# Kernel tuning notes

Measured on AMD Instinct MI355X. Metric: run time of the kernel, lower is better.

## Reference

```python
import jax, jax.numpy as jnp
import numpy as np

B, C, H, W = 16, 512, 32, 32
NH, HD = 8, 64
CTX_DIM, L = 768, 512
EPS = 1e-5


def setup_inputs() -> dict:
    key = jax.random.key(0)
    ks = jax.random.split(key, 10)
    x = jax.random.normal(ks[0], (B, C, H, W), dtype=jnp.float32)
    context = jax.random.normal(ks[1], (B, L, CTX_DIM), dtype=jnp.float32)
    context_mask = jax.random.randint(ks[2], (B, L), 0, 2).astype(bool)
    context_mask = context_mask.at[:, 0].set(True)  # guarantee >=1 valid key per row
    s = 0.02
    ln_w = jnp.ones((C,), jnp.float32)
    ln_b = jnp.zeros((C,), jnp.float32)
    Wq = jax.random.normal(ks[3], (C, C), jnp.float32) * s
    Wk = jax.random.normal(ks[4], (C, C), jnp.float32) * s
    Wv = jax.random.normal(ks[5], (C, C), jnp.float32) * s
    Wo = jax.random.normal(ks[6], (C, C), jnp.float32) * s
    Wctx = jax.random.normal(ks[7], (C, CTX_DIM), jnp.float32) * s
    return {"x": x, "context": context, "context_mask": context_mask,
            "ln_w": ln_w, "ln_b": ln_b, "Wq": Wq, "Wk": Wk, "Wv": Wv,
            "Wo": Wo, "Wctx": Wctx}


def _layernorm(x, w, b):
    mu = jnp.mean(x, axis=-1, keepdims=True)
    var = jnp.mean(jnp.square(x - mu), axis=-1, keepdims=True)
    return (x - mu) * jax.lax.rsqrt(var + EPS) * w + b


def reference(x, context, context_mask, ln_w, ln_b, Wq, Wk, Wv, Wo, Wctx):
    b, c, h, w = x.shape
    n = h * w
    hidden = x.reshape(b, c, n).transpose(0, 2, 1)          # [b, n, c]
    hidden_norm = _layernorm(hidden, ln_w, ln_b)
    ctx = jnp.einsum('bld,cd->blc', context, Wctx)          # context_proj

    q = jnp.einsum('bnc,ec->bne', hidden_norm, Wq).reshape(b, n, NH, HD).transpose(0, 2, 1, 3)
    k = jnp.einsum('blc,ec->ble', ctx, Wk).reshape(b, -1, NH, HD).transpose(0, 2, 1, 3)
    v = jnp.einsum('blc,ec->ble', ctx, Wv).reshape(b, -1, NH, HD).transpose(0, 2, 1, 3)

    scale = HD ** -0.5
    scores = jnp.einsum('bhnd,bhld->bhnl', q, k) * scale    # [b,H,n,L]
    mask4 = context_mask[:, None, None, :]                  # [b,1,1,L]
    scores = jnp.where(mask4, scores, -jnp.inf)
    all_invalid = ~jnp.any(mask4, axis=-1, keepdims=True)   # [b,1,1,1]
    scores = jnp.where(all_invalid, 0.0, scores)
    attn = jax.nn.softmax(scores, axis=-1)
    attn = jnp.where(mask4, attn, 0.0)
    attn = jnp.where(all_invalid, 0.0, attn)

    out = jnp.einsum('bhnl,bhld->bhnd', attn, v)            # [b,H,n,hd]
    out = out.transpose(0, 2, 1, 3).reshape(b, n, c)
    out = jnp.einsum('bnc,ec->bne', out, Wo)
    out = out + hidden
    return out.transpose(0, 2, 1).reshape(b, c, h, w)
```

## Files before the change

kernel.cpp:

```cpp
#include <hip/hip_runtime.h>

#define B_   16
#define C_   512
#define N_   1024
#define L_   512
#define CTX_ 768
#define NH_  8
#define HD_  64
#define EPS_ 1e-5f

typedef short bfrag  __attribute__((ext_vector_type(8)));
typedef short bfrag4 __attribute__((ext_vector_type(4)));
typedef float f32x4  __attribute__((ext_vector_type(4)));

__device__ __forceinline__ ushort f2bf(float f) {
  union { float f; unsigned u; } v; v.f = f;
  unsigned r = v.u + 0x7fffu + ((v.u >> 16) & 1u);
  return (ushort)(r >> 16);
}

__device__ __forceinline__ f32x4 mfma16(bfrag a, bfrag b, f32x4 c) {
  return __builtin_amdgcn_mfma_f32_16x16x32_bf16(a, b, c, 0, 0, 0);
}
__device__ __forceinline__ f32x4 mfma16k16(bfrag4 a, bfrag4 b, f32x4 c) {
  return __builtin_amdgcn_mfma_f32_16x16x16bf16_1k(a, b, c, 0, 0, 0);
}
__device__ __forceinline__ unsigned cvt_pk_bf16(float lo, float hi) {
  unsigned d;
  asm("v_cvt_pk_bf16_f32 %0, %1, %2" : "=v"(d) : "v"(lo), "v"(hi));
  return d;
}

__device__ __forceinline__ void g2l16(const ushort* g, ushort* l) {
  __builtin_amdgcn_global_load_lds(
      (const __attribute__((address_space(1))) void*)g,
      (__attribute__((address_space(3))) void*)l, 16, 0, 0);
}

__global__ __launch_bounds__(256) void cast5_kernel(
    const float* __restrict__ s0, const float* __restrict__ s1,
    const float* __restrict__ s2, const float* __restrict__ s3,
    const float* __restrict__ s4,
    ushort* __restrict__ d0, ushort* __restrict__ d1, ushort* __restrict__ d2,
    ushort* __restrict__ d3, ushort* __restrict__ d4) {
  int i = blockIdx.x * 256 + threadIdx.x;
  const float* src; ushort* dst; int off;
  if      (i < 98304)  { src = s0; dst = d0; off = i; }
  else if (i < 163840) { src = s1; dst = d1; off = i - 98304; }
  else if (i < 229376) { src = s2; dst = d2; off = i - 163840; }
  else if (i < 294912) { src = s3; dst = d3; off = i - 229376; }
  else                 { src = s4; dst = d4; off = i - 294912; }
  float4 vv = ((const float4*)src)[off];
  ushort4 o;
  o.x = f2bf(vv.x); o.y = f2bf(vv.y); o.z = f2bf(vv.z); o.w = f2bf(vv.w);
  ((ushort4*)dst)[off] = o;
}

__global__ __launch_bounds__(1024) void ln_stats(const float* __restrict__ x,
                                                 float* __restrict__ mu_out,
                                                 float* __restrict__ rs_out) {
  const int b  = blockIdx.x;
  const int n0 = blockIdx.y * 64;
  const int tid = threadIdx.x;
  const int nx = tid & 63, cg = tid >> 6;
  const float* xb = x + (size_t)b * C_ * N_;

  float s = 0.f, s2 = 0.f;
  for (int c = cg; c < C_; c += 16) {
    float v = xb[(size_t)c * N_ + n0 + nx];
    s += v; s2 += v * v;
  }
  __shared__ float red[2][16][64];
  red[0][cg][nx] = s; red[1][cg][nx] = s2;
  __syncthreads();
  if (cg == 0) {
    float ss = 0.f, ss2 = 0.f;
#pragma unroll
    for (int i = 0; i < 16; ++i) { ss += red[0][i][nx]; ss2 += red[1][i][nx]; }
    float m  = ss * (1.f / C_);
    float var = ss2 * (1.f / C_) - m * m;
    mu_out[(size_t)b * N_ + n0 + nx] = m;
    rs_out[(size_t)b * N_ + n0 + nx] = rsqrtf(var + EPS_);
  }
}

__device__ __forceinline__ void gemm_core(const ushort* __restrict__ A,
                                          const ushort* __restrict__ W,
                                          int K, ushort* la, ushort* lb,
                                          f32x4 acc[4][4],
                                          int tid, int wm, int we, int col, int rg) {
  const int lane = tid & 63, w = tid >> 6;
  const int rloc = lane >> 2, pt = lane & 3;
  const int pts = pt ^ ((rloc >> 1) & 3);
  const int qsel = (rg ^ ((col >> 1) & 3)) * 8;

  for (int k0 = 0; k0 < K; k0 += 32) {
#pragma unroll
    for (int c = 0; c < 2; ++c) {
      const int chunk = w + c * 4;
      const int row = chunk * 16 + rloc;
      g2l16(A + (size_t)row * K + k0 + pts * 8, la + chunk * 512);
      g2l16(W + (size_t)row * K + k0 + pts * 8, lb + chunk * 512);
    }
    __syncthreads();
    bfrag af[4], bf[4];
#pragma unroll
    for (int i = 0; i < 4; ++i) {
      af[i] = *(const bfrag*)&la[(wm + i * 16 + col) * 32 + qsel];
      bf[i] = *(const bfrag*)&lb[(we + i * 16 + col) * 32 + qsel];
    }
#pragma unroll
    for (int i = 0; i < 4; ++i)
#pragma unroll
      for (int j = 0; j < 4; ++j)
        acc[i][j] = mfma16(af[i], bf[j], acc[i][j]);
    __syncthreads();
  }
}

__global__ __launch_bounds__(256) void gemm_kv(const ushort* __restrict__ A,
                                               const ushort* __restrict__ Wk,
                                               const ushort* __restrict__ Wv,
                                               ushort* __restrict__ Ko,
                                               ushort* __restrict__ Vt_g) {
  __shared__ ushort la[128 * 32];
  __shared__ ushort lb[128 * 32];
  __shared__ float T[16][132];
  const int isv = blockIdx.y >> 2;
  const ushort* W = isv ? Wv : Wk;
  const int m0 = blockIdx.x * 128, e0 = (blockIdx.y & 3) * 128;
  const int tid = threadIdx.x, lane = tid & 63, w = tid >> 6;
  const int wm = (w >> 1) * 64, we = (w & 1) * 64;
  const int col = lane & 15, rg = lane >> 4;

  f32x4 acc[4][4] = {};
  gemm_core(A + (size_t)m0 * C_, W + (size_t)e0 * C_, C_, la, lb, acc, tid, wm, we, col, rg);

  if (!isv) {
#pragma unroll
    for (int i = 0; i < 4; ++i)
#pragma unroll
      for (int j = 0; j < 4; ++j)
#pragma unroll
        for (int r = 0; r < 4; ++r)
          Ko[(size_t)(m0 + wm + i * 16 + rg * 4 + r) * 512 + e0 + we + j * 16 + col] =
              f2bf(acc[i][j][r]);
  } else {
    const int b = m0 >> 9, l0 = m0 & 511;
#pragma unroll
    for (int g = 0; g < 8; ++g) {
      if ((w & 1) == (g >> 2)) {
        const int j = g & 3;
#pragma unroll
        for (int i = 0; i < 4; ++i)
          *(f32x4*)&T[col][wm + i * 16 + rg * 4] = acc[i][j];
      }
      __syncthreads();
      const int n = tid & 127;
      for (int cc = tid >> 7; cc < 16; cc += 2) {
        const int e = e0 + g * 16 + cc;
        Vt_g[((size_t)b * 512 + e) * 512 + l0 + n] = f2bf(T[cc][n]);
      }
      __syncthreads();
    }
  }
}

__global__ __launch_bounds__(256) void gemm_res(const ushort* __restrict__ A,
                                                const ushort* __restrict__ W,
                                                const float* __restrict__ x,
                                                float* __restrict__ out) {
  __shared__ ushort la[128 * 32];
  __shared__ ushort lb[128 * 32];
  __shared__ float T[16][132];
  const int m0 = blockIdx.x * 128, e0 = blockIdx.y * 128;
  const int tid = threadIdx.x, lane = tid & 63, w = tid >> 6;
  const int wm = (w >> 1) * 64, we = (w & 1) * 64;
  const int col = lane & 15, rg = lane >> 4;

  f32x4 acc[4][4] = {};
  gemm_core(A + (size_t)m0 * C_, W + (size_t)e0 * C_, C_, la, lb, acc, tid, wm, we, col, rg);

  const int b = m0 >> 10, n0l = m0 & 1023;
#pragma unroll
  for (int g = 0; g < 8; ++g) {
    if ((w & 1) == (g >> 2)) {
      const int j = g & 3;
#pragma unroll
      for (int i = 0; i < 4; ++i)
        *(f32x4*)&T[col][wm + i * 16 + rg * 4] = acc[i][j];
    }
    __syncthreads();
    const int n = tid & 127;
    for (int cc = tid >> 7; cc < 16; cc += 2) {
      const int c = e0 + g * 16 + cc;
      const size_t idx = (size_t)b * C_ * N_ + (size_t)c * N_ + n0l + n;
      out[idx] = T[cc][n] + x[idx];
    }
    __syncthreads();
  }
}

__global__ __launch_bounds__(256) void gemm_ctxlnq(
    const float* __restrict__ context, const ushort* __restrict__ Wctxb,
    ushort* __restrict__ ctxo,
    const float* __restrict__ x, const float* __restrict__ mu,
    const float* __restrict__ rs, const float* __restrict__ lnw,
    const float* __restrict__ lnb, const ushort* __restrict__ Wqb,
    ushort* __restrict__ qo) {
  __shared__ ushort la[128 * 40];
  __shared__ ushort lb[128 * 40];
  const int bid = blockIdx.x;
  const int tid = threadIdx.x, lane = tid & 63, w = tid >> 6;
  const int wm = (w >> 1) * 64, we = (w & 1) * 64;
  const int col = lane & 15, rg = lane >> 4;
  const int srow = tid >> 1, sh = (tid & 1) * 16;

  f32x4 acc[4][4] = {};

  if (bid < 256) {
    const int m0 = (bid >> 2) * 128, e0 = (bid & 3) * 128;
    const int K = CTX_;
    for (int k0 = 0; k0 < K; k0 += 32) {
      {
        const float* ap = &context[(size_t)(m0 + srow) * K + k0 + sh];
        float4 f0 = ((const float4*)ap)[0];
        float4 f1 = ((const float4*)ap)[1];
        float4 f2 = ((const float4*)ap)[2];
        float4 f3 = ((const float4*)ap)[3];
        union { int4 v; ushort u[8]; } p0, p1;
        p0.u[0] = f2bf(f0.x); p0.u[1] = f2bf(f0.y); p0.u[2] = f2bf(f0.z); p0.u[3] = f2bf(f0.w);
        p0.u[4] = f2bf(f1.x); p0.u[5] = f2bf(f1.y); p0.u[6] = f2bf(f1.z); p0.u[7] = f2bf(f1.w);
        p1.u[0] = f2bf(f2.x); p1.u[1] = f2bf(f2.y); p1.u[2] = f2bf(f2.z); p1.u[3] = f2bf(f2.w);
        p1.u[4] = f2bf(f3.x); p1.u[5] = f2bf(f3.y); p1.u[6] = f2bf(f3.z); p1.u[7] = f2bf(f3.w);
        *(int4*)&la[srow * 40 + sh]     = p0.v;
        *(int4*)&la[srow * 40 + sh + 8] = p1.v;
        const ushort* wp = &Wctxb[(size_t)(e0 + srow) * K + k0 + sh];
        *(int4*)&lb[srow * 40 + sh]     = *(const int4*)wp;
        *(int4*)&lb[srow * 40 + sh + 8] = *(const int4*)(wp + 8);
      }
      __syncthreads();
      bfrag af[4], bf[4];
#pragma unroll
      for (int i = 0; i < 4; ++i) {
        af[i] = *(const bfrag*)&la[(wm + i * 16 + col) * 40 + rg * 8];
        bf[i] = *(const bfrag*)&lb[(we + i * 16 + col) * 40 + rg * 8];
      }
#pragma unroll
      for (int i = 0; i < 4; ++i)
#pragma unroll
        for (int j = 0; j < 4; ++j)
          acc[i][j] = mfma16(af[i], bf[j], acc[i][j]);
      __syncthreads();
    }
#pragma unroll
    for (int i = 0; i < 4; ++i)
#pragma unroll
      for (int j = 0; j < 4; ++j)
#pragma unroll
        for (int r = 0; r < 4; ++r)
          ctxo[(size_t)(m0 + wm + i * 16 + rg * 4 + r) * 512 + e0 + we + j * 16 + col] =
              f2bf(acc[i][j][r]);
  } else {
    const int b2 = bid - 256;
    const int m0 = (b2 >> 2) * 128, e0 = (b2 & 3) * 128;
    const int b = m0 >> 10, n0l = m0 & 1023;
    const int nloc = tid & 127, chalf = (tid >> 7) * 16;

    const float muv = mu[(size_t)b * N_ + n0l + nloc];
    const float rsv = rs[(size_t)b * N_ + n0l + nloc];
    const float nmr = -muv * rsv;
    const float* xb = x + (size_t)b * C_ * N_ + n0l + nloc;

    for (int k0 = 0; k0 < C_; k0 += 32) {
      {
        union { int4 v[2]; ushort u[16]; } pk;
#pragma unroll
        for (int i = 0; i < 16; ++i) {
          const int c = k0 + chalf + i;
          const float xv = xb[(size_t)c * N_];
          const float t = fmaf(xv, rsv, nmr);
          pk.u[i] = f2bf(fmaf(t, lnw[c], lnb[c]));
        }
        *(int4*)&la[nloc * 40 + chalf]     = pk.v[0];
        *(int4*)&la[nloc * 40 + chalf + 8] = pk.v[1];
        const ushort* wp = &Wqb[(size_t)(e0 + srow) * C_ + k0 + sh];
        *(int4*)&lb[srow * 40 + sh]     = *(const int4*)wp;
        *(int4*)&lb[srow * 40 + sh + 8] = *(const int4*)(wp + 8);
      }
      __syncthreads();
      bfrag af[4], bf[4];
#pragma unroll
      for (int i = 0; i < 4; ++i) {
        af[i] = *(const bfrag*)&la[(wm + i * 16 + col) * 40 + rg * 8];
        bf[i] = *(const bfrag*)&lb[(we + i * 16 + col) * 40 + rg * 8];
      }
#pragma unroll
      for (int i = 0; i < 4; ++i)
#pragma unroll
        for (int j = 0; j < 4; ++j)
          acc[i][j] = mfma16(af[i], bf[j], acc[i][j]);
      __syncthreads();
    }
#pragma unroll
    for (int i = 0; i < 4; ++i)
#pragma unroll
      for (int j = 0; j < 4; ++j)
#pragma unroll
        for (int r = 0; r < 4; ++r)
          qo[(size_t)(m0 + wm + i * 16 + rg * 4 + r) * 512 + e0 + we + j * 16 + col] =
              f2bf(acc[i][j][r]);
  }
}

__global__ __launch_bounds__(256) void attn_mfma(const ushort* __restrict__ q,
                                                 const ushort* __restrict__ k,
                                                 const ushort* __restrict__ vt,
                                                 const int* __restrict__ mask,
                                                 ushort* __restrict__ o) {
  __shared__ ushort Kl[2][64 * 72];
  __shared__ ushort Vt[2][64 * 72];
  __shared__ float mlb[2][64];

  const int lin = blockIdx.x;
  const int hb = lin & 127, qb = lin >> 7;
  const int h = hb & 7, b = hb >> 3;
  const int q0 = qb * 128;
  const int tid = threadIdx.x, lane = tid & 63, w = tid >> 6;
  const int col = lane & 15, rg = lane >> 4;
  const int wq = w * 32;
  const float C1 = 0.18033688011112042f;

  bfrag qf[2][2];
#pragma unroll
  for (int mi = 0; mi < 2; ++mi)
#pragma unroll
    for (int kc = 0; kc < 2; ++kc)
      qf[mi][kc] = *(const bfrag*)
          &q[((size_t)b * N_ + q0 + wq + mi * 16 + col) * C_ + h * HD_ + kc * 32 + rg * 8];

  f32x4 oa[2][4] = {};
  float l_part[2] = {0.f, 0.f};

  {
#pragma unroll
    for (int it = 0; it < 2; ++it) {
      const int idx = it * 256 + tid;
      const int key = idx >> 3, part = idx & 7;
      *(int4*)&Kl[0][key * 72 + part * 8] =
          *(const int4*)&k[((size_t)b * L_ + key) * C_ + h * HD_ + part * 8];
    }
#pragma unroll
    for (int it = 0; it < 2; ++it) {
      const int idx = it * 256 + tid;
      const int d = idx >> 3, k8 = (idx & 7) * 8;
      *(int4*)&Vt[0][d * 72 + k8] =
          *(const int4*)&vt[((size_t)b * 512 + h * HD_ + d) * 512 + k8];
    }
    if (tid < 64) mlb[0][tid] = mask[b * L_ + tid] ? 0.f : -1e30f;
  }
  __syncthreads();

  for (int t = 0; t < 8; ++t) {
    const int cur = t & 1;
    int4 kreg[2];
    int4 vreg[2];
    float mreg = 0.f;
    if (t < 7) {
      const int l0n = (t + 1) * 64;
#pragma unroll
      for (int it = 0; it < 2; ++it) {
        const int idx = it * 256 + tid;
        const int key = idx >> 3, part = idx & 7;
        kreg[it] = *(const int4*)&k[((size_t)b * L_ + l0n + key) * C_ + h * HD_ + part * 8];
      }
#pragma unroll
      for (int it = 0; it < 2; ++it) {
        const int idx = it * 256 + tid;
        const int d = idx >> 3, k8 = (idx & 7) * 8;
        vreg[it] = *(const int4*)&vt[((size_t)b * 512 + h * HD_ + d) * 512 + l0n + k8];
      }
      if (tid < 64) mreg = mask[b * L_ + l0n + tid] ? 0.f : -1e30f;
    }

    const ushort* Kc = &Kl[cur][0];
    const ushort* Vc = &Vt[cur][0];
    f32x4 s2[2][4] = {};
#pragma unroll
    for (int kc = 0; kc < 2; ++kc) {
      bfrag kf[4];
#pragma unroll
      for (int ni = 0; ni < 4; ++ni)
        kf[ni] = *(const bfrag*)&Kc[(ni * 16 + col) * 72 + kc * 32 + rg * 8];
#pragma unroll
      for (int mi = 0; mi < 2; ++mi)
#pragma unroll
        for (int ni = 0; ni < 4; ++ni)
          s2[mi][ni] = mfma16(kf[ni], qf[mi][kc], s2[mi][ni]);
    }
    bfrag4 pf[2][4];
#pragma unroll
    for (int ni = 0; ni < 4; ++ni) {
      const f32x4 bias4 = *(const f32x4*)&mlb[cur][ni * 16 + rg * 4];
#pragma unroll
      for (int mi = 0; mi < 2; ++mi) {
        const float p0 = exp2f(fmaf(s2[mi][ni][0], C1, bias4[0]));
        const float p1 = exp2f(fmaf(s2[mi][ni][1], C1, bias4[1]));
        const float p2 = exp2f(fmaf(s2[mi][ni][2], C1, bias4[2]));
        const float p3 = exp2f(fmaf(s2[mi][ni][3], C1, bias4[3]));
        l_part[mi] += (p0 + p1) + (p2 + p3);
        union { bfrag4 v; unsigned u[2]; } pk;
        pk.u[0] = cvt_pk_bf16(p0, p1);
        pk.u[1] = cvt_pk_bf16(p2, p3);
        pf[mi][ni] = pk.v;
      }
    }
#pragma unroll
    for (int ni = 0; ni < 4; ++ni) {
      bfrag4 vf[4];
#pragma unroll
      for (int di = 0; di < 4; ++di)
        vf[di] = *(const bfrag4*)&Vc[(di * 16 + col) * 72 + ni * 16 + rg * 4];
#pragma unroll
      for (int mi = 0; mi < 2; ++mi)
#pragma unroll
        for (int di = 0; di < 4; ++di)
          oa[mi][di] = mfma16k16(pf[mi][ni], vf[di], oa[mi][di]);
    }

    if (t < 7) {
      const int nb = cur ^ 1;
#pragma unroll
      for (int it = 0; it < 2; ++it) {
        const int idx = it * 256 + tid;
        const int key = idx >> 3, part = idx & 7;
        *(int4*)&Kl[nb][key * 72 + part * 8] = kreg[it];
      }
#pragma unroll
      for (int it = 0; it < 2; ++it) {
        const int idx = it * 256 + tid;
        const int d = idx >> 3, k8 = (idx & 7) * 8;
        *(int4*)&Vt[nb][d * 72 + k8] = vreg[it];
      }
      if (tid < 64) mlb[nb][tid] = mreg;
    }
    __syncthreads();
  }

  float linv[2][4];
#pragma unroll
  for (int mi = 0; mi < 2; ++mi) {
    float l = l_part[mi];
    l += __shfl_xor(l, 16);
    l += __shfl_xor(l, 32);
#pragma unroll
    for (int r = 0; r < 4; ++r) {
      int lv = __builtin_amdgcn_ds_bpermute((rg * 4 + r) * 4, __float_as_int(l));
      linv[mi][r] = 1.f / __int_as_float(lv);
    }
  }
#pragma unroll
  for (int mi = 0; mi < 2; ++mi)
#pragma unroll
    for (int r = 0; r < 4; ++r) {
      const size_t row = (size_t)b * N_ + q0 + wq + mi * 16 + rg * 4 + r;
#pragma unroll
      for (int di = 0; di < 4; ++di)
        o[row * C_ + h * HD_ + di * 16 + col] = f2bf(oa[mi][di][r] * linv[mi][r]);
    }
}

extern "C" void kernel_launch(void* const* d_in, const int* in_sizes, int n_in,
                              void* d_out, int out_size, void* d_ws, size_t ws_size,
                              hipStream_t stream) {
  (void)in_sizes; (void)n_in; (void)out_size; (void)ws_size;
  const float* x       = (const float*)d_in[0];
  const float* context = (const float*)d_in[1];
  const int*   mask    = (const int*)d_in[2];
  const float* ln_w    = (const float*)d_in[3];
  const float* ln_b    = (const float*)d_in[4];
  const float* Wq      = (const float*)d_in[5];
  const float* Wk      = (const float*)d_in[6];
  const float* Wv      = (const float*)d_in[7];
  const float* Wo      = (const float*)d_in[8];
  const float* Wctx    = (const float*)d_in[9];

  char* wsb = (char*)d_ws;
  ushort* qb    = (ushort*)(wsb + 0);
  ushort* kb    = (ushort*)(wsb + 16777216);
  ushort* vb    = (ushort*)(wsb + 25165824);
  ushort* atto  = (ushort*)(wsb + 33554432);
  ushort* ctx   = (ushort*)(wsb + 50331648);
  ushort* wctxb = (ushort*)(wsb + 58720256);
  ushort* wqb   = (ushort*)(wsb + 59506688);
  ushort* wkb   = (ushort*)(wsb + 60030976);
  ushort* wvb   = (ushort*)(wsb + 60555264);
  ushort* wob   = (ushort*)(wsb + 61079552);
  float*  mub   = (float*)(wsb + 61603840);
  float*  rsb   = (float*)(wsb + 61669376);

  cast5_kernel<<<1408, 256, 0, stream>>>(Wctx, Wq, Wk, Wv, Wo,
                                         wctxb, wqb, wkb, wvb, wob);
  ln_stats<<<dim3(B_, N_ / 64), 1024, 0, stream>>>(x, mub, rsb);
  gemm_ctxlnq<<<768, 256, 0, stream>>>(context, wctxb, ctx,
                                       x, mub, rsb, ln_w, ln_b, wqb, qb);
  gemm_kv<<<dim3(64, 8), 256, 0, stream>>>(ctx, wkb, wvb, kb, vb);
  attn_mfma<<<1024, 256, 0, stream>>>(qb, kb, vb, mask, atto);
  gemm_res<<<dim3(128, 4), 256, 0, stream>>>(atto, wob, x, (float*)d_out);
}
```

Baseline: 157.5 us.

## Materialize bf16 context and LayerNorm output before a shared GEMM core

Context is cast to bf16 in the weight-cast kernel, and the LayerNorm kernel now writes the normalized, transposed hidden state as bf16 rather than only statistics. The context and Q projections then reuse the shared gemm_core path with direct global-to-LDS loads, instead of converting fp32 and applying the norm inside the GEMM tile loaders. This removes strided fp32 loads of x and redundant per-tile conversion inside the GEMM. In exchange it adds extra global writes and reads of bf16 intermediates (about 16 MB hidden state plus 12 MB context).

```diff
diff --git a/kernel.cpp b/kernel.cpp
--- a/kernel.cpp
+++ b/kernel.cpp
@@ -37,28 +37,30 @@
       (__attribute__((address_space(3))) void*)l, 16, 0, 0);
 }
 
-__global__ __launch_bounds__(256) void cast5_kernel(
+__global__ __launch_bounds__(256) void cast6_kernel(
     const float* __restrict__ s0, const float* __restrict__ s1,
     const float* __restrict__ s2, const float* __restrict__ s3,
-    const float* __restrict__ s4,
+    const float* __restrict__ s4, const float* __restrict__ s5,
     ushort* __restrict__ d0, ushort* __restrict__ d1, ushort* __restrict__ d2,
-    ushort* __restrict__ d3, ushort* __restrict__ d4) {
+    ushort* __restrict__ d3, ushort* __restrict__ d4, ushort* __restrict__ d5) {
   int i = blockIdx.x * 256 + threadIdx.x;
   const float* src; ushort* dst; int off;
-  if      (i < 98304)  { src = s0; dst = d0; off = i; }
-  else if (i < 163840) { src = s1; dst = d1; off = i - 98304; }
-  else if (i < 229376) { src = s2; dst = d2; off = i - 163840; }
-  else if (i < 294912) { src = s3; dst = d3; off = i - 229376; }
-  else                 { src = s4; dst = d4; off = i - 294912; }
+  if      (i < 1572864) { src = s0; dst = d0; off = i; }
+  else if (i < 1671168) { src = s1; dst = d1; off = i - 1572864; }
+  else if (i < 1736704) { src = s2; dst = d2; off = i - 1671168; }
+  else if (i < 1802240) { src = s3; dst = d3; off = i - 1736704; }
+  else if (i < 1867776) { src = s4; dst = d4; off = i - 1802240; }
+  else                  { src = s5; dst = d5; off = i - 1867776; }
   float4 vv = ((const float4*)src)[off];
   ushort4 o;
   o.x = f2bf(vv.x); o.y = f2bf(vv.y); o.z = f2bf(vv.z); o.w = f2bf(vv.w);
   ((ushort4*)dst)[off] = o;
 }
 
-__global__ __launch_bounds__(1024) void ln_stats(const float* __restrict__ x,
-                                                 float* __restrict__ mu_out,
-                                                 float* __restrict__ rs_out) {
+__global__ __launch_bounds__(1024) void ln_kernel(const float* __restrict__ x,
+                                                  const float* __restrict__ w,
+                                                  const float* __restrict__ bia,
+                                                  ushort* __restrict__ hn) {
   const int b  = blockIdx.x;
   const int n0 = blockIdx.y * 64;
   const int tid = threadIdx.x;
@@ -71,16 +73,33 @@
     s += v; s2 += v * v;
   }
   __shared__ float red[2][16][64];
+  __shared__ float mean[64], rstd[64];
   red[0][cg][nx] = s; red[1][cg][nx] = s2;
   __syncthreads();
   if (cg == 0) {
     float ss = 0.f, ss2 = 0.f;
 #pragma unroll
     for (int i = 0; i < 16; ++i) { ss += red[0][i][nx]; ss2 += red[1][i][nx]; }
-    float m  = ss * (1.f / C_);
-    float var = ss2 * (1.f / C_) - m * m;
-    mu_out[(size_t)b * N_ + n0 + nx] = m;
-    rs_out[(size_t)b * N_ + n0 + nx] = rsqrtf(var + EPS_);
+    float mu  = ss * (1.f / C_);
+    float var = ss2 * (1.f / C_) - mu * mu;
+    mean[nx] = mu;
+    rstd[nx] = rsqrtf(var + EPS_);
+  }
+  __syncthreads();
+
+  __shared__ float tile[64][65];
+  for (int ct = 0; ct < 8; ++ct) {
+    const int c0 = ct * 64;
+    for (int cy = cg; cy < 64; cy += 16)
+      tile[cy][nx] = xb[(size_t)(c0 + cy) * N_ + n0 + nx];
+    __syncthreads();
+    const int cx = tid & 63, ng = tid >> 6;
+    const float wv = w[c0 + cx], bv = bia[c0 + cx];
+    for (int ny = ng; ny < 64; ny += 16) {
+      float val = (tile[cx][ny] - mean[ny]) * rstd[ny] * wv + bv;
+      hn[((size_t)b * N_ + n0 + ny) * C_ + c0 + cx] = f2bf(val);
+    }
+    __syncthreads();
   }
 }
 
@@ -116,6 +135,42 @@
         acc[i][j] = mfma16(af[i], bf[j], acc[i][j]);
     __syncthreads();
   }
+}
+
+__global__ __launch_bounds__(256) void gemm_ctxq(const ushort* __restrict__ ctxb,
+                                                 const ushort* __restrict__ Wctxb,
+                                                 ushort* __restrict__ ctxo,
+                                                 const ushort* __restrict__ hn,
+                                                 const ushort* __restrict__ Wqb,
+                                                 ushort* __restrict__ qo) {
+  __shared__ ushort la[128 * 32];
+  __shared__ ushort lb[128 * 32];
+  const int bid = blockIdx.x;
+  const int tid = threadIdx.x, lane = tid & 63, w = tid >> 6;
+  const int wm = (w >> 1) * 64, we = (w & 1) * 64;
+  const int col = lane & 15, rg = lane >> 4;
+
+  const ushort* A; const ushort* W; ushort* out; int K, m0, e0;
+  if (bid < 256) {
+    m0 = (bid >> 2) * 128; e0 = (bid & 3) * 128;
+    A = ctxb; W = Wctxb; out = ctxo; K = CTX_;
+  } else {
+    const int b2 = bid - 256;
+    m0 = (b2 >> 2) * 128; e0 = (b2 & 3) * 128;
+    A = hn; W = Wqb; out = qo; K = C_;
+  }
+
+  f32x4 acc[4][4] = {};
+  gemm_core(A + (size_t)m0 * K, W + (size_t)e0 * K, K, la, lb, acc, tid, wm, we, col, rg);
+
+#pragma unroll
+  for (int i = 0; i < 4; ++i)
+#pragma unroll
+    for (int j = 0; j < 4; ++j)
+#pragma unroll
+      for (int r = 0; r < 4; ++r)
+        out[(size_t)(m0 + wm + i * 16 + rg * 4 + r) * 512 + e0 + we + j * 16 + col] =
+            f2bf(acc[i][j][r]);
 }
 
 __global__ __launch_bounds__(256) void gemm_kv(const ushort* __restrict__ A,
@@ -201,118 +256,6 @@
   }
 }
 
-__global__ __launch_bounds__(256) void gemm_ctxlnq(
-    const float* __restrict__ context, const ushort* __restrict__ Wctxb,
-    ushort* __restrict__ ctxo,
-    const float* __restrict__ x, const float* __restrict__ mu,
-    const float* __restrict__ rs, const float* __restrict__ lnw,
-    const float* __restrict__ lnb, const ushort* __restrict__ Wqb,
-    ushort* __restrict__ qo) {
-  __shared__ ushort la[128 * 40];
-  __shared__ ushort lb[128 * 40];
-  const int bid = blockIdx.x;
-  const int tid = threadIdx.x, lane = tid & 63, w = tid >> 6;
-  const int wm = (w >> 1) * 64, we = (w & 1) * 64;
-  const int col = lane & 15, rg = lane >> 4;
-  const int srow = tid >> 1, sh = (tid & 1) * 16;
-
-  f32x4 acc[4][4] = {};
-
-  if (bid < 256) {
-    const int m0 = (bid >> 2) * 128, e0 = (bid & 3) * 128;
-    const int K = CTX_;
-    for (int k0 = 0; k0 < K; k0 += 32) {
-      {
-        const float* ap = &context[(size_t)(m0 + srow) * K + k0 + sh];
-        float4 f0 = ((const float4*)ap)[0];
-        float4 f1 = ((const float4*)ap)[1];
-        float4 f2 = ((const float4*)ap)[2];
-        float4 f3 = ((const float4*)ap)[3];
-        union { int4 v; ushort u[8]; } p0, p1;
-        p0.u[0] = f2bf(f0.x); p0.u[1] = f2bf(f0.y); p0.u[2] = f2bf(f0.z); p0.u[3] = f2bf(f0.w);
-        p0.u[4] = f2bf(f1.x); p0.u[5] = f2bf(f1.y); p0.u[6] = f2bf(f1.z); p0.u[7] = f2bf(f1.w);
-        p1.u[0] = f2bf(f2.x); p1.u[1] = f2bf(f2.y); p1.u[2] = f2bf(f2.z); p1.u[3] = f2bf(f2.w);
-        p1.u[4] = f2bf(f3.x); p1.u[5] = f2bf(f3.y); p1.u[6] = f2bf(f3.z); p1.u[7] = f2bf(f3.w);
-        *(int4*)&la[srow * 40 + sh]     = p0.v;
-        *(int4*)&la[srow * 40 + sh + 8] = p1.v;
-        const ushort* wp = &Wctxb[(size_t)(e0 + srow) * K + k0 + sh];
-        *(int4*)&lb[srow * 40 + sh]     = *(const int4*)wp;
-        *(int4*)&lb[srow * 40 + sh + 8] = *(const int4*)(wp + 8);
-      }
-      __syncthreads();
-      bfrag af[4], bf[4];
-#pragma unroll
-      for (int i = 0; i < 4; ++i) {
-        af[i] = *(const bfrag*)&la[(wm + i * 16 + col) * 40 + rg * 8];
-        bf[i] = *(const bfrag*)&lb[(we + i * 16 + col) * 40 + rg * 8];
-      }
-#pragma unroll
-      for (int i = 0; i < 4; ++i)
-#pragma unroll
-        for (int j = 0; j < 4; ++j)
-          acc[i][j] = mfma16(af[i], bf[j], acc[i][j]);
-      __syncthreads();
-    }
-#pragma unroll
-    for (int i = 0; i < 4; ++i)
-#pragma unroll
-      for (int j = 0; j < 4; ++j)
-#pragma unroll
-        for (int r = 0; r < 4; ++r)
-          ctxo[(size_t)(m0 + wm + i * 16 + rg * 4 + r) * 512 + e0 + we + j * 16 + col] =
-              f2bf(acc[i][j][r]);
-  } else {
-    const int b2 = bid - 256;
-    const int m0 = (b2 >> 2) * 128, e0 = (b2 & 3) * 128;
-    const int b = m0 >> 10, n0l = m0 & 1023;
-    const int nloc = tid & 127, chalf = (tid >> 7) * 16;
-
-    const float muv = mu[(size_t)b * N_ + n0l + nloc];
-    const float rsv = rs[(size_t)b * N_ + n0l + nloc];
-    const float nmr = -muv * rsv;
-    const float* xb = x + (size_t)b * C_ * N_ + n0l + nloc;
-
-    for (int k0 = 0; k0 < C_; k0 += 32) {
-      {
-        union { int4 v[2]; ushort u[16]; } pk;
-#pragma unroll
-        for (int i = 0; i < 16; ++i) {
-          const int c = k0 + chalf + i;
-          const float xv = xb[(size_t)c * N_];
-          const float t = fmaf(xv, rsv, nmr);
-          pk.u[i] = f2bf(fmaf(t, lnw[c], lnb[c]));
-        }
-        *(int4*)&la[nloc * 40 + chalf]     = pk.v[0];
-        *(int4*)&la[nloc * 40 + chalf + 8] = pk.v[1];
-        const ushort* wp = &Wqb[(size_t)(e0 + srow) * C_ + k0 + sh];
-        *(int4*)&lb[srow * 40 + sh]     = *(const int4*)wp;
-        *(int4*)&lb[srow * 40 + sh + 8] = *(const int4*)(wp + 8);
-      }
-      __syncthreads();
-      bfrag af[4], bf[4];
-#pragma unroll
-      for (int i = 0; i < 4; ++i) {
-        af[i] = *(const bfrag*)&la[(wm + i * 16 + col) * 40 + rg * 8];
-        bf[i] = *(const bfrag*)&lb[(we + i * 16 + col) * 40 + rg * 8];
-      }
-#pragma unroll
-      for (int i = 0; i < 4; ++i)
-#pragma unroll
-        for (int j = 0; j < 4; ++j)
-          acc[i][j] = mfma16(af[i], bf[j], acc[i][j]);
-      __syncthreads();
-    }
-#pragma unroll
-    for (int i = 0; i < 4; ++i)
-#pragma unroll
-      for (int j = 0; j < 4; ++j)
-#pragma unroll
-        for (int r = 0; r < 4; ++r)
-          qo[(size_t)(m0 + wm + i * 16 + rg * 4 + r) * 512 + e0 + we + j * 16 + col] =
-              f2bf(acc[i][j][r]);
-  }
-}
-
 __global__ __launch_bounds__(256) void attn_mfma(const ushort* __restrict__ q,
                                                  const ushort* __restrict__ k,
                                                  const ushort* __restrict__ vt,
@@ -496,14 +439,13 @@
   ushort* wkb   = (ushort*)(wsb + 60030976);
   ushort* wvb   = (ushort*)(wsb + 60555264);
   ushort* wob   = (ushort*)(wsb + 61079552);
-  float*  mub   = (float*)(wsb + 61603840);
-  float*  rsb   = (float*)(wsb + 61669376);
-
-  cast5_kernel<<<1408, 256, 0, stream>>>(Wctx, Wq, Wk, Wv, Wo,
-                                         wctxb, wqb, wkb, wvb, wob);
-  ln_stats<<<dim3(B_, N_ / 64), 1024, 0, stream>>>(x, mub, rsb);
-  gemm_ctxlnq<<<768, 256, 0, stream>>>(context, wctxb, ctx,
-                                       x, mub, rsb, ln_w, ln_b, wqb, qb);
+  ushort* hn    = (ushort*)(wsb + 61603840);
+  ushort* ctxb  = (ushort*)(wsb + 78381056);
+
+  cast6_kernel<<<7552, 256, 0, stream>>>(context, Wctx, Wq, Wk, Wv, Wo,
+                                         ctxb, wctxb, wqb, wkb, wvb, wob);
+  ln_kernel<<<dim3(B_, N_ / 64), 1024, 0, stream>>>(x, ln_w, ln_b, hn);
+  gemm_ctxq<<<768, 256, 0, stream>>>(ctxb, wctxb, ctx, hn, wqb, qb);
   gemm_kv<<<dim3(64, 8), 256, 0, stream>>>(ctx, wkb, wvb, kb, vb);
   attn_mfma<<<1024, 256, 0, stream>>>(qb, kb, vb, mask, atto);
   gemm_res<<<dim3(128, 4), 256, 0, stream>>>(atto, wob, x, (float*)d_out);
```

Result: faster. 148.2 us (-5.9%).
